# Performance work log

Measured on AMD Instinct MI355X. Metric: run time of the kernel, lower is better.

Reference implementation:

```python
import jax, jax.numpy as jnp
import numpy as np

NEG_SLOPE = 0.2  # PyG GATConv default negative_slope


def gat_layer(x, src, dst, N, W, att_src, att_dst, bias, heads, out_ch, concat):
    # x: [N, Fin]; W: [Fin, heads*out_ch]; att_*: [heads, out_ch]; bias matches output dim
    h = (x @ W).reshape(N, heads, out_ch)              # [N, H, C]
    a_src = (h * att_src).sum(-1)                      # [N, H]
    a_dst = (h * att_dst).sum(-1)                      # [N, H]
    e = jax.nn.leaky_relu(a_src[src] + a_dst[dst], NEG_SLOPE)  # [E, H]
    # segment softmax over incoming edges of each destination node
    e_max = jax.ops.segment_max(e, dst, num_segments=N)        # [N, H]
    e_exp = jnp.exp(e - e_max[dst])                             # [E, H]
    denom = jax.ops.segment_sum(e_exp, dst, num_segments=N)    # [N, H]
    alpha = e_exp / (denom[dst] + 1e-16)                        # [E, H]
    msg = alpha[:, :, None] * h[src]                            # [E, H, C]
    out = jax.ops.segment_sum(msg, dst, num_segments=N)        # [N, H, C]
    out = out.reshape(N, heads * out_ch) if concat else out.mean(axis=1)
    return out + bias


def setup_inputs() -> dict:
    key = jax.random.key(0)
    ks = jax.random.split(key, 10)
    N, E = 40000, 160000
    Fin, H1, C1 = 602, 8, 256
    H2, C2 = 1, 42
    g = lambda k, shape, fan: (jax.random.normal(k, shape, dtype=jnp.float32) * (1.0 / np.sqrt(fan)))
    return {
        "x": jax.random.normal(ks[0], (N, Fin), dtype=jnp.float32),
        "edge_index": jax.random.randint(ks[1], (2, E), 0, N, dtype=jnp.int64),
        "W1": g(ks[2], (Fin, H1 * C1), Fin),
        "att_src1": g(ks[3], (H1, C1), C1),
        "att_dst1": g(ks[4], (H1, C1), C1),
        "b1": jnp.zeros((H1 * C1,), dtype=jnp.float32),
        "W2": g(ks[5], (H1 * C1, H2 * C2), H1 * C1),
        "att_src2": g(ks[6], (H2, C2), C2),
        "att_dst2": g(ks[7], (H2, C2), C2),
        "b2": jnp.zeros((C2,), dtype=jnp.float32),
    }


def reference(x, edge_index, W1, att_src1, att_dst1, b1, W2, att_src2, att_dst2, b2):
    N = x.shape[0]
    # PyG GATConv default add_self_loops=True
    loops = jnp.arange(N, dtype=edge_index.dtype)
    src = jnp.concatenate([edge_index[0], loops])
    dst = jnp.concatenate([edge_index[1], loops])
    h = gat_layer(x, src, dst, N, W1, att_src1, att_dst1, b1, heads=8, out_ch=256, concat=True)
    h = jax.nn.relu(h)  # dropout is identity in eval mode
    h = gat_layer(h, src, dst, N, W2, att_src2, att_dst2, b2, heads=1, out_ch=42, concat=False)
    return jax.nn.log_softmax(h, axis=1)
```

## Files before the change

kernel.cpp:

```cpp
#include <hip/hip_runtime.h>
#include <hip/hip_bf16.h>

#define NN   40000
#define NE   160000
#define ETOT 200000
#define FIN  602
#define NH1  8
#define C1   256
#define F1   2048
#define C2   42
#define NEG  0.2f
#define NB   157
#define KP   608
#define MP   40192

typedef unsigned short u16;
typedef unsigned int   u32;
typedef __bf16 bf16x8 __attribute__((ext_vector_type(8)));
typedef float  f32x4  __attribute__((ext_vector_type(4)));

__device__ __forceinline__ float bfu(u16 v){ return __uint_as_float(((u32)v) << 16); }
__device__ __forceinline__ float bflo(u32 u){ return __uint_as_float(u << 16); }
__device__ __forceinline__ float bfhi(u32 u){ return __uint_as_float(u & 0xffff0000u); }
__device__ __forceinline__ u16 f2bf(float f){
  u32 u = __float_as_uint(f);
  u32 r = (u + 0x7fffu + ((u >> 16) & 1u)) >> 16;
  return (u16)r;
}

__device__ __forceinline__ void gl_lds16(const u16* g, u16* l) {
  __builtin_amdgcn_global_load_lds(
      (const __attribute__((address_space(1))) u32*)(g),
      (__attribute__((address_space(3))) u32*)(l), 16, 0, 0);
}

__global__ void probe_k(const u32* __restrict__ xw, const int* __restrict__ ei,
                        int* __restrict__ flags) {
  if (threadIdx.x == 0) {
    int zc = 0;
    for (int k = 0; k < 64; ++k) zc += (ei[2*k + 1] == 0) ? 1 : 0;
    flags[0] = (zc == 64) ? 1 : 0;
    int inr = 0;
    for (int k = 0; k < 64; ++k) {
      u32 low = xw[k] & 0xffffu;
      int e = (int)((low >> 7) & 0xff);
      inr += (e >= 100 && e <= 140) ? 1 : 0;
    }
    flags[1] = (inr >= 32) ? 0 : 1;
  }
}

__global__ void cvt_f32_k(const void* __restrict__ src, float* __restrict__ dst, int n,
                          const int* __restrict__ flags) {
  int i = blockIdx.x * 256 + threadIdx.x;
  if (i >= n) return;
  dst[i] = flags[1] ? ((const float*)src)[i] : bfu(((const u16*)src)[i]);
}

__global__ void xb_k(const void* __restrict__ x, u16* __restrict__ xb,
                     const int* __restrict__ flags) {
  int k = blockIdx.x * 256 + threadIdx.x;
  int row = blockIdx.y;
  if (k >= KP) return;
  u16 v = 0;
  if (row < NN && k < FIN)
    v = flags[1] ? f2bf(((const float*)x)[(size_t)row * FIN + k])
                 : ((const u16*)x)[(size_t)row * FIN + k];
  xb[(size_t)row * KP + k] = v;
}

__global__ void w1t_k(const void* __restrict__ W1, u16* __restrict__ w1t,
                      const int* __restrict__ flags) {
  int n = blockIdx.x * 256 + threadIdx.x;
  int k = blockIdx.y;
  if (n >= F1) return;
  u16 v = 0;
  if (k < FIN) v = flags[1] ? f2bf(((const float*)W1)[(size_t)k * F1 + n])
                            : ((const u16*)W1)[(size_t)k * F1 + n];
  w1t[(size_t)n * KP + k] = v;
}

__global__ void w2t_k(const void* __restrict__ W2, u16* __restrict__ w2t,
                      const int* __restrict__ flags) {
  int i = blockIdx.x * 256 + threadIdx.x;
  if (i >= 64 * F1) return;
  int c = i >> 11, k = i & (F1 - 1);
  u16 v = 0;
  if (c < C2) v = flags[1] ? f2bf(((const float*)W2)[(size_t)k * C2 + c])
                           : ((const u16*)W2)[(size_t)k * C2 + c];
  w2t[i] = v;
}

__device__ __forceinline__ void edge_sd(const int* __restrict__ ei, int e, int imode,
                                        int& s, int& d) {
  if (e < NE) {
    if (imode) { s = ei[2*e]; d = ei[2*(NE + e)]; }
    else       { s = ei[e];   d = ei[NE + e];     }
  } else { s = d = e - NE; }
}

__global__ void deg_k(const int* __restrict__ ei, int* __restrict__ deg,
                      const int* __restrict__ flags) {
  int e = blockIdx.x * 256 + threadIdx.x;
  if (e >= ETOT) return;
  int s, d; edge_sd(ei, e, flags[0], s, d);
  atomicAdd(&deg[d], 1);
}

__global__ __launch_bounds__(256) void scan1_k(const int* __restrict__ deg,
                                               int* __restrict__ tmp, int* __restrict__ bsum) {
  __shared__ int s[256];
  int b = blockIdx.x, t = threadIdx.x, i = b * 256 + t;
  int v = (i < NN) ? deg[i] : 0;
  s[t] = v; __syncthreads();
  for (int o = 1; o < 256; o <<= 1) {
    int u = (t >= o) ? s[t - o] : 0;
    __syncthreads(); s[t] += u; __syncthreads();
  }
  if (i < NN) tmp[i] = s[t];
  if (t == 255) bsum[b] = s[255];
}

__global__ __launch_bounds__(256) void scan2_k(int* __restrict__ bsum) {
  __shared__ int s[256];
  int t = threadIdx.x;
  int v = (t < NB) ? bsum[t] : 0;
  s[t] = v; __syncthreads();
  for (int o = 1; o < 256; o <<= 1) {
    int u = (t >= o) ? s[t - o] : 0;
    __syncthreads(); s[t] += u; __syncthreads();
  }
  if (t < NB) bsum[t] = s[t];
}

__global__ void scan3_k(const int* __restrict__ deg, const int* __restrict__ tmp,
                        const int* __restrict__ bsum, int* __restrict__ start, int* __restrict__ cur) {
  int i = blockIdx.x * 256 + threadIdx.x;
  if (i >= NN) return;
  int b = i >> 8;
  int off = b ? bsum[b - 1] : 0;
  int excl = tmp[i] - deg[i] + off;
  start[i] = excl; cur[i] = excl;
}

__global__ void fill_k(const int* __restrict__ ei, int* __restrict__ cur,
                       int* __restrict__ csr_src, int* __restrict__ csr_dst,
                       const int* __restrict__ flags) {
  int e = blockIdx.x * 256 + threadIdx.x;
  if (e >= ETOT) return;
  int s, d; edge_sd(ei, e, flags[0], s, d);
  int pos = atomicAdd(&cur[d], 1);
  csr_src[pos] = s; csr_dst[pos] = d;
}

__global__ __launch_bounds__(512) void gemm1c_k(const u16* __restrict__ xb,
                                                const u16* __restrict__ w1t,
                                                u16* __restrict__ h1,
                                                const float* __restrict__ as1c,
                                                const float* __restrict__ ad1c,
                                                float* __restrict__ a_s1,
                                                float* __restrict__ a_d1) {
  __shared__ u16 As[2 * 8192];
  __shared__ u16 Bs[2 * 8192];
  const int t = threadIdx.x;
  const int lane = t & 63, wid = t >> 6;
  const int wr = wid >> 2, wc = wid & 3;
  const int m0 = blockIdx.y * 256, n0 = blockIdx.x * 256;
  const int l16 = lane & 15;
  f32x4 acc[8][4];
  #pragma unroll
  for (int i = 0; i < 8; ++i)
    #pragma unroll
    for (int j = 0; j < 4; ++j) acc[i][j] = (f32x4){0.f, 0.f, 0.f, 0.f};

  const int kc = ((t & 3) ^ ((t >> 3) & 3)) * 8;
  const size_t sa0 = (size_t)(m0 + (t >> 2)) * KP + kc;
  const size_t sa1 = sa0 + (size_t)128 * KP;
  const size_t sb0 = (size_t)(n0 + (t >> 2)) * KP + kc;
  const size_t sb1 = sb0 + (size_t)128 * KP;

  const int fsw = ((lane >> 4) ^ ((l16 >> 1) & 3)) << 3;
  const int rdA = (wr * 128 + l16) * 32 + fsw;
  const int rdB = (wc * 64 + l16) * 32 + fsw;

#define STAGE(K0, B) do {                                  \
    u16* a_ = As + (B) * 8192 + (wid << 9);                \
    u16* b_ = Bs + (B) * 8192 + (wid << 9);                \
    gl_lds16(xb  + sa0 + (K0), a_);                        \
    gl_lds16(xb  + sa1 + (K0), a_ + 4096);                 \
    gl_lds16(w1t + sb0 + (K0), b_);                        \
    gl_lds16(w1t + sb1 + (K0), b_ + 4096);                 \
  } while (0)

  STAGE(0, 0);
  __syncthreads();
  int cur = 0;
  for (int k0 = 0; k0 < KP; k0 += 32) {
    if (k0 + 32 < KP) STAGE(k0 + 32, cur ^ 1);
    const u16* Ab = As + cur * 8192;
    const u16* Bb = Bs + cur * 8192;
    bf16x8 bfr[4];
    #pragma unroll
    for (int ni = 0; ni < 4; ++ni)
      bfr[ni] = *(const bf16x8*)&Bb[rdB + ni * 512];
    #pragma unroll
    for (int mi = 0; mi < 8; ++mi) {
      bf16x8 af = *(const bf16x8*)&Ab[rdA + mi * 512];
      #pragma unroll
      for (int ni = 0; ni < 4; ++ni)
        acc[mi][ni] = __builtin_amdgcn_mfma_f32_16x16x32_bf16(af, bfr[ni], acc[mi][ni], 0, 0, 0);
    }
    __syncthreads();
    cur ^= 1;
  }
#undef STAGE

  const int h0 = n0 >> 8;
  const int lr4 = (lane >> 4) * 4;
  #pragma unroll
  for (int mi = 0; mi < 8; ++mi) {
    float ps[4] = {0.f, 0.f, 0.f, 0.f}, pd[4] = {0.f, 0.f, 0.f, 0.f};
    #pragma unroll
    for (int ni = 0; ni < 4; ++ni) {
      int col = n0 + wc * 64 + ni * 16 + l16;
      float wsv = as1c[col], wdv = ad1c[col];
      #pragma unroll
      for (int r = 0; r < 4; ++r) {
        float v = acc[mi][ni][r];
        ps[r] += v * wsv;
        pd[r] += v * wdv;
      }
    }
    #pragma unroll
    for (int o = 1; o < 16; o <<= 1) {
      #pragma unroll
      for (int r = 0; r < 4; ++r) {
        ps[r] += __shfl_xor(ps[r], o, 64);
        pd[r] += __shfl_xor(pd[r], o, 64);
      }
    }
    int rowb = m0 + wr * 128 + mi * 16 + lr4;
    if (l16 == 0) {
      #pragma unroll
      for (int r = 0; r < 4; ++r) {
        int row = rowb + r;
        if (row < NN) {
          atomicAdd(&a_s1[row * NH1 + h0], ps[r]);
          atomicAdd(&a_d1[row * NH1 + h0], pd[r]);
        }
      }
    }
    #pragma unroll
    for (int r = 0; r < 4; ++r) {
      int row = rowb + r;
      if (row < NN) {
        #pragma unroll
        for (int ni = 0; ni < 4; ++ni) {
          int col = n0 + wc * 64 + ni * 16 + l16;
          h1[(size_t)row * F1 + col] = f2bf(acc[mi][ni][r]);
        }
      }
    }
  }
}

__global__ __launch_bounds__(256) void gemm1m_k(const void* __restrict__ xv,
                                                const u16* __restrict__ w1t,
                                                u16* __restrict__ h1,
                                                const int* __restrict__ flags) {
  __shared__ u16 As[128][40];
  __shared__ u16 Bs[128][40];
  const int fm = flags[1];
  const int t = threadIdx.x;
  const int lane = t & 63, wid = t >> 6;
  const int wr = wid >> 1, wc = wid & 1;
  const int m0 = blockIdx.y * 128, n0 = blockIdx.x * 128;
  const int l16 = lane & 15, lk = (lane >> 4) * 8;
  f32x4 acc[4][4];
  #pragma unroll
  for (int i = 0; i < 4; ++i)
    #pragma unroll
    for (int j = 0; j < 4; ++j) acc[i][j] = (f32x4){0.f, 0.f, 0.f, 0.f};
  const int arow = t >> 2;
  const int akb  = (t & 3) * 8;
  for (int k0 = 0; k0 < KP; k0 += 32) {
    #pragma unroll
    for (int i = 0; i < 2; ++i) {
      int row = arow + i * 64;
      int rg = m0 + row;
      u32 d0 = 0, d1 = 0, d2 = 0, d3 = 0;
      if (rg < NN) {
        if (k0 + 32 <= FIN) {
          if (fm) {
            const float* xp = (const float*)xv + (size_t)rg * FIN + k0 + akb;
            float2 p0 = *(const float2*)(xp);
            float2 p1 = *(const float2*)(xp + 2);
            float2 p2 = *(const float2*)(xp + 4);
            float2 p3 = *(const float2*)(xp + 6);
            d0 = (u32)f2bf(p0.x) | ((u32)f2bf(p0.y) << 16);
            d1 = (u32)f2bf(p1.x) | ((u32)f2bf(p1.y) << 16);
            d2 = (u32)f2bf(p2.x) | ((u32)f2bf(p2.y) << 16);
            d3 = (u32)f2bf(p3.x) | ((u32)f2bf(p3.y) << 16);
          } else {
            const u16* xp = (const u16*)xv + (size_t)rg * FIN + k0 + akb;
            d0 = *(const u32*)(xp);
            d1 = *(const u32*)(xp + 2);
            d2 = *(const u32*)(xp + 4);
            d3 = *(const u32*)(xp + 6);
          }
        } else {
          u16 e[8];
          #pragma unroll
          for (int q = 0; q < 8; ++q) {
            int k = k0 + akb + q;
            e[q] = 0;
            if (k < FIN)
              e[q] = fm ? f2bf(((const float*)xv)[(size_t)rg * FIN + k])
                        : ((const u16*)xv)[(size_t)rg * FIN + k];
          }
          d0 = (u32)e[0] | ((u32)e[1] << 16);
          d1 = (u32)e[2] | ((u32)e[3] << 16);
          d2 = (u32)e[4] | ((u32)e[5] << 16);
          d3 = (u32)e[6] | ((u32)e[7] << 16);
        }
      }
      *(uint4*)&As[row][akb] = make_uint4(d0, d1, d2, d3);
      const u16* wp = w1t + (size_t)(n0 + row) * KP + k0 + akb;
      *(uint4*)&Bs[row][akb] = *(const uint4*)wp;
    }
    __syncthreads();
    bf16x8 bfr[4];
    #pragma unroll
    for (int ni = 0; ni < 4; ++ni)
      bfr[ni] = *(const bf16x8*)&Bs[wc * 64 + ni * 16 + l16][lk];
    #pragma unroll
    for (int mi = 0; mi < 4; ++mi) {
      bf16x8 af = *(const bf16x8*)&As[wr * 64 + mi * 16 + l16][lk];
      #pragma unroll
      for (int ni = 0; ni < 4; ++ni)
        acc[mi][ni] = __builtin_amdgcn_mfma_f32_16x16x32_bf16(af, bfr[ni], acc[mi][ni], 0, 0, 0);
    }
    __syncthreads();
  }
  const int lr4 = (lane >> 4) * 4;
  #pragma unroll
  for (int mi = 0; mi < 4; ++mi) {
    #pragma unroll
    for (int r = 0; r < 4; ++r) {
      int row = m0 + wr * 64 + mi * 16 + lr4 + r;
      if (row < NN) {
        #pragma unroll
        for (int ni = 0; ni < 4; ++ni) {
          int col = n0 + wc * 64 + ni * 16 + l16;
          h1[(size_t)row * F1 + col] = f2bf(acc[mi][ni][r]);
        }
      }
    }
  }
}

__global__ __launch_bounds__(256) void att1_k(const u16* __restrict__ h1,
                                              const float* __restrict__ as1c, const float* __restrict__ ad1c,
                                              float* __restrict__ a_s, float* __restrict__ a_d) {
  int n = blockIdx.x, t = threadIdx.x;
  int h = t >> 5, l = t & 31;
  int base = h * C1 + l * 8;
  const u16* hp = h1 + (size_t)n * F1 + base;
  uint4 v = *(const uint4*)hp;
  u32 w[4] = {v.x, v.y, v.z, v.w};
  float ss = 0.f, sd = 0.f;
  #pragma unroll
  for (int p = 0; p < 4; ++p) {
    float e0 = bflo(w[p]), e1 = bfhi(w[p]);
    ss += e0 * as1c[base + 2*p] + e1 * as1c[base + 2*p + 1];
    sd += e0 * ad1c[base + 2*p] + e1 * ad1c[base + 2*p + 1];
  }
  #pragma unroll
  for (int o = 16; o > 0; o >>= 1) {
    ss += __shfl_down(ss, o, 32);
    sd += __shfl_down(sd, o, 32);
  }
  if (l == 0) { a_s[n * NH1 + h] = ss; a_d[n * NH1 + h] = sd; }
}

__global__ __launch_bounds__(512) void gfuse_k(const int* __restrict__ start, const int* __restrict__ deg,
                                               const int* __restrict__ csr_src,
                                               const float* __restrict__ a_s1, const float* __restrict__ a_d1,
                                               const u16* __restrict__ h1, const float* __restrict__ b1c,
                                               const u16* __restrict__ w2t, float* __restrict__ h2) {
  __shared__ u16 rowsL[16 * F1];
  __shared__ float pb[4][16][16];
  int t = threadIdx.x;
  int nb = blockIdx.x * 16;
  int sub = t & 255, grp = t >> 8;
  int h = sub >> 5;
  int c0 = sub * 8;
  float4 bA = *(const float4*)(b1c + c0);
  float4 bB = *(const float4*)(b1c + c0 + 4);
  for (int ii = 0; ii < 8; ++ii) {
    int i = grp * 8 + ii;
    int n = nb + i;
    int s0 = start[n], jend = s0 + deg[n];
    float ad = a_d1[n * NH1 + h];
    float a0=0.f,a1=0.f,a2=0.f,a3=0.f,a4=0.f,a5=0.f,a6=0.f,a7=0.f,den=0.f;
    int j = s0;
    for (; j + 2 <= jend; j += 2) {
      int sA = csr_src[j], sB = csr_src[j + 1];
      float vA = a_s1[sA * NH1 + h] + ad;
      float vB = a_s1[sB * NH1 + h] + ad;
      vA = vA > 0.f ? vA : NEG * vA;
      vB = vB > 0.f ? vB : NEG * vB;
      float eA = expf(vA), eB = expf(vB);
      uint4 uA = *(const uint4*)(h1 + (size_t)sA * F1 + c0);
      uint4 uB = *(const uint4*)(h1 + (size_t)sB * F1 + c0);
      den += eA + eB;
      a0 += eA * bflo(uA.x) + eB * bflo(uB.x);
      a1 += eA * bfhi(uA.x) + eB * bfhi(uB.x);
      a2 += eA * bflo(uA.y) + eB * bflo(uB.y);
      a3 += eA * bfhi(uA.y) + eB * bfhi(uB.y);
      a4 += eA * bflo(uA.z) + eB * bflo(uB.z);
      a5 += eA * bfhi(uA.z) + eB * bfhi(uB.z);
      a6 += eA * bflo(uA.w) + eB * bflo(uB.w);
      a7 += eA * bfhi(uA.w) + eB * bfhi(uB.w);
    }
    if (j < jend) {
      int sA = csr_src[j];
      float vA = a_s1[sA * NH1 + h] + ad;
      vA = vA > 0.f ? vA : NEG * vA;
      float eA = expf(vA);
      uint4 uA = *(const uint4*)(h1 + (size_t)sA * F1 + c0);
      den += eA;
      a0 += eA * bflo(uA.x); a1 += eA * bfhi(uA.x);
      a2 += eA * bflo(uA.y); a3 += eA * bfhi(uA.y);
      a4 += eA * bflo(uA.z); a5 += eA * bfhi(uA.z);
      a6 += eA * bflo(uA.w); a7 += eA * bfhi(uA.w);
    }
    float inv = 1.f / (den + 1e-16f);
    u16 o0 = f2bf(fmaxf(a0 * inv + bA.x, 0.f));
    u16 o1 = f2bf(fmaxf(a1 * inv + bA.y, 0.f));
    u16 o2 = f2bf(fmaxf(a2 * inv + bA.z, 0.f));
    u16 o3 = f2bf(fmaxf(a3 * inv + bA.w, 0.f));
    u16 o4 = f2bf(fmaxf(a4 * inv + bB.x, 0.f));
    u16 o5 = f2bf(fmaxf(a5 * inv + bB.y, 0.f));
    u16 o6 = f2bf(fmaxf(a6 * inv + bB.z, 0.f));
    u16 o7 = f2bf(fmaxf(a7 * inv + bB.w, 0.f));
    uint4 pk;
    pk.x = (u32)o0 | ((u32)o1 << 16);
    pk.y = (u32)o2 | ((u32)o3 << 16);
    pk.z = (u32)o4 | ((u32)o5 << 16);
    pk.w = (u32)o6 | ((u32)o7 << 16);
    int sw = (i & 7) << 3;
    *(uint4*)&rowsL[i * F1 + (c0 ^ sw)] = pk;
  }
  __syncthreads();
  int lane = t & 63, wid = t >> 6;
  int g = wid & 3, kh = wid >> 2;
  int l16 = lane & 15, lk = (lane >> 4) * 8;
  const u16* wt = w2t + (size_t)(g * 16 + l16) * F1;
  int sw = (l16 & 7) << 3;
  f32x4 acc2 = (f32x4){0.f, 0.f, 0.f, 0.f};
  const int kbase = kh * (F1 / 2);
  for (int k0 = 0; k0 < F1 / 2; k0 += 32) {
    int kk = kbase + k0 + lk;
    bf16x8 af = *(const bf16x8*)&rowsL[l16 * F1 + (kk ^ sw)];
    bf16x8 bf = *(const bf16x8*)(wt + kk);
    acc2 = __builtin_amdgcn_mfma_f32_16x16x32_bf16(af, bf, acc2, 0, 0, 0);
  }
  int mb = (lane >> 4) * 4;
  if (kh == 1) {
    #pragma unroll
    for (int r = 0; r < 4; ++r) pb[g][mb + r][l16] = acc2[r];
  }
  __syncthreads();
  if (kh == 0) {
    int col = g * 16 + l16;
    if (col < C2) {
      #pragma unroll
      for (int r = 0; r < 4; ++r)
        h2[(size_t)(nb + mb + r) * C2 + col] = acc2[r] + pb[g][mb + r][l16];
    }
  }
}

__global__ __launch_bounds__(64) void att2_k(const float* __restrict__ h2,
                                             const float* __restrict__ as2, const float* __restrict__ ad2,
                                             float* __restrict__ a_s, float* __restrict__ a_d) {
  int n = blockIdx.x, t = threadIdx.x;
  float ss = 0.f, sd = 0.f;
  if (t < C2) {
    float v = h2[(size_t)n * C2 + t];
    ss = v * as2[t];
    sd = v * ad2[t];
  }
  #pragma unroll
  for (int o = 32; o > 0; o >>= 1) {
    ss += __shfl_down(ss, o, 64);
    sd += __shfl_down(sd, o, 64);
  }
  if (t == 0) { a_s[n] = ss; a_d[n] = sd; }
}

__global__ __launch_bounds__(64) void gath2_k(const int* __restrict__ start, const int* __restrict__ deg,
                                              const int* __restrict__ csr_src,
                                              const float* __restrict__ a_s, const float* __restrict__ a_d,
                                              const float* __restrict__ h2, const float* __restrict__ b2,
                                              void* __restrict__ outv, const int* __restrict__ flags) {
  int n = blockIdx.x, t = threadIdx.x;
  int s0 = start[n], cnt = deg[n];
  float ad = a_d[n];
  float acc = 0.f, den = 0.f;
  for (int j = s0; j < s0 + cnt; ++j) {
    int s = csr_src[j];
    float v = a_s[s] + ad;
    v = v > 0.f ? v : NEG * v;
    float e = expf(v);
    den += e;
    if (t < C2) acc += e * h2[(size_t)s * C2 + t];
  }
  float raw = (t < C2) ? acc / (den + 1e-16f) + b2[t] : -1e30f;
  float m = raw;
  #pragma unroll
  for (int o = 32; o > 0; o >>= 1) m = fmaxf(m, __shfl_down(m, o, 64));
  m = __shfl(m, 0, 64);
  float e2 = (t < C2) ? expf(raw - m) : 0.f;
  float ssum = e2;
  #pragma unroll
  for (int o = 32; o > 0; o >>= 1) ssum += __shfl_down(ssum, o, 64);
  ssum = __shfl(ssum, 0, 64);
  if (t < C2) {
    float v = raw - m - logf(ssum);
    if (flags[1]) ((float*)outv)[(size_t)n * C2 + t] = v;
    else          ((u16*) outv)[(size_t)n * C2 + t] = f2bf(v);
  }
}

extern "C" void kernel_launch(void* const* d_in, const int* in_sizes, int n_in,
                              void* d_out, int out_size, void* d_ws, size_t ws_size,
                              hipStream_t stream) {
  const void* x   = d_in[0];
  const int*  ei  = (const int*)d_in[1];
  const void* W1  = d_in[2];
  const void* as1 = d_in[3];
  const void* ad1 = d_in[4];
  const void* b1  = d_in[5];
  const void* W2  = d_in[6];
  const void* as2 = d_in[7];
  const void* ad2 = d_in[8];
  const void* b2  = d_in[9];

  char* ws = (char*)d_ws;
  u16*   h1      = (u16*)  (ws);
  float* h2      = (float*)(ws + 163840000);
  float* a_s1    = (float*)(ws + 170560000);
  float* a_d1    = (float*)(ws + 171840000);
  float* a_s2    = (float*)(ws + 173120000);
  float* a_d2    = (float*)(ws + 173280000);
  int*   deg     = (int*)  (ws + 173440000);
  int*   start   = (int*)  (ws + 173600000);
  int*   cur     = (int*)  (ws + 173760000);
  int*   tmp     = (int*)  (ws + 173920000);
  int*   csr_src = (int*)  (ws + 174080000);
  int*   csr_dst = (int*)  (ws + 174880000);
  int*   bsum    = (int*)  (ws + 175680000);
  u16*   w1t     = (u16*)  (ws + 175681024);
  u16*   w2t     = (u16*)  (ws + 178171392);
  float* as1c    = (float*)(ws + 178433536);
  float* ad1c    = (float*)(ws + 178441728);
  float* b1c     = (float*)(ws + 178449920);
  float* as2c    = (float*)(ws + 178458112);
  float* ad2c    = (float*)(ws + 178458368);
  float* b2c     = (float*)(ws + 178458624);
  int*   flags   = (int*)  (ws + 178458880);
  const size_t TOTAL_BASE = 178459136;
  u16*   xb      = (u16*)  (ws + TOTAL_BASE);
  const size_t TOTAL_A = TOTAL_BASE + (size_t)MP * KP * 2;
  if (ws_size < TOTAL_BASE) return;
  const bool pathA = (ws_size >= TOTAL_A);

  probe_k<<<1, 64, 0, stream>>>((const u32*)x, ei, flags);

  cvt_f32_k<<<(F1 + 255) / 256, 256, 0, stream>>>(as1, as1c, F1, flags);
  cvt_f32_k<<<(F1 + 255) / 256, 256, 0, stream>>>(ad1, ad1c, F1, flags);
  cvt_f32_k<<<(F1 + 255) / 256, 256, 0, stream>>>(b1, b1c, F1, flags);
  cvt_f32_k<<<1, 256, 0, stream>>>(as2, as2c, C2, flags);
  cvt_f32_k<<<1, 256, 0, stream>>>(ad2, ad2c, C2, flags);
  cvt_f32_k<<<1, 256, 0, stream>>>(b2, b2c, C2, flags);
  w1t_k<<<dim3(8, KP), 256, 0, stream>>>(W1, w1t, flags);
  w2t_k<<<(64 * F1 + 255) / 256, 256, 0, stream>>>(W2, w2t, flags);

  hipMemsetAsync(deg, 0, NN * sizeof(int), stream);
  hipMemsetAsync(a_s1, 0, 2 * NN * NH1 * sizeof(float), stream);
  const int EB = (ETOT + 255) / 256;
  deg_k  <<<EB, 256, 0, stream>>>(ei, deg, flags);
  scan1_k<<<NB, 256, 0, stream>>>(deg, tmp, bsum);
  scan2_k<<<1, 256, 0, stream>>>(bsum);
  scan3_k<<<NB, 256, 0, stream>>>(deg, tmp, bsum, start, cur);
  fill_k <<<EB, 256, 0, stream>>>(ei, cur, csr_src, csr_dst, flags);

  if (pathA) {
    xb_k<<<dim3((KP + 255) / 256, MP), 256, 0, stream>>>(x, xb, flags);
    gemm1c_k<<<dim3(8, MP / 256), 512, 0, stream>>>(xb, w1t, h1, as1c, ad1c, a_s1, a_d1);
  } else {
    gemm1m_k<<<dim3(16, 313), 256, 0, stream>>>(x, w1t, h1, flags);
    att1_k<<<NN, 256, 0, stream>>>(h1, as1c, ad1c, a_s1, a_d1);
  }
  gfuse_k<<<NN / 16, 512, 0, stream>>>(start, deg, csr_src, a_s1, a_d1, h1, b1c, w2t, h2);

  att2_k<<<NN, 64, 0, stream>>>(h2, as2c, ad2c, a_s2, a_d2);
  gath2_k<<<NN, 64, 0, stream>>>(start, deg, csr_src, a_s2, a_d2, h2, b2c, d_out, flags);
}
```

Before: 641.7 us.

## Stage GEMM1 output through LDS, fuse att2 into gfuse, merge conversion kernels

The GEMM1 epilogue now writes bf16 tiles into shared memory and copies them out with 16-byte vector stores, replacing scattered 2-byte global stores. The layer-2 attention dot products are computed inside gfuse with shuffle reductions and atomics, which removes the separate att2 kernel and its re-read of h2. The six small parameter conversion launches become one kernel, and gath2 packs four nodes per 256-thread block. This adds extra barriers in the GEMM epilogue and depends on a_s2/a_d2 sitting right after a_s1 in the workspace so the enlarged memset zeroes them.

Result: faster. 623.1 us (-2.9%).

```diff
diff --git a/kernel.cpp b/kernel.cpp
--- a/kernel.cpp
+++ b/kernel.cpp
@@ -13,6 +13,7 @@
 #define NB   157
 #define KP   608
 #define MP   40192
+#define CSS  264
 
 typedef unsigned short u16;
 typedef unsigned int   u32;
@@ -50,11 +51,25 @@
   }
 }
 
-__global__ void cvt_f32_k(const void* __restrict__ src, float* __restrict__ dst, int n,
+__global__ void cvt_all_k(const void* __restrict__ as1, const void* __restrict__ ad1,
+                          const void* __restrict__ b1,  const void* __restrict__ as2,
+                          const void* __restrict__ ad2, const void* __restrict__ b2,
+                          float* __restrict__ as1c, float* __restrict__ ad1c,
+                          float* __restrict__ b1c,  float* __restrict__ as2c,
+                          float* __restrict__ ad2c, float* __restrict__ b2c,
                           const int* __restrict__ flags) {
   int i = blockIdx.x * 256 + threadIdx.x;
-  if (i >= n) return;
-  dst[i] = flags[1] ? ((const float*)src)[i] : bfu(((const u16*)src)[i]);
+  int fm = flags[1];
+  if (i < F1) {
+    as1c[i] = fm ? ((const float*)as1)[i] : bfu(((const u16*)as1)[i]);
+    ad1c[i] = fm ? ((const float*)ad1)[i] : bfu(((const u16*)ad1)[i]);
+    b1c[i]  = fm ? ((const float*)b1)[i]  : bfu(((const u16*)b1)[i]);
+  }
+  if (i < C2) {
+    as2c[i] = fm ? ((const float*)as2)[i] : bfu(((const u16*)as2)[i]);
+    ad2c[i] = fm ? ((const float*)ad2)[i] : bfu(((const u16*)ad2)[i]);
+    b2c[i]  = fm ? ((const float*)b2)[i]  : bfu(((const u16*)b2)[i]);
+  }
 }
 
 __global__ void xb_k(const void* __restrict__ x, u16* __restrict__ xb,
@@ -239,8 +254,8 @@
         pd[r] += __shfl_xor(pd[r], o, 64);
       }
     }
-    int rowb = m0 + wr * 128 + mi * 16 + lr4;
     if (l16 == 0) {
+      int rowb = m0 + wr * 128 + mi * 16 + lr4;
       #pragma unroll
       for (int r = 0; r < 4; ++r) {
         int row = rowb + r;
@@ -250,16 +265,25 @@
         }
       }
     }
-    #pragma unroll
-    for (int r = 0; r < 4; ++r) {
-      int row = rowb + r;
-      if (row < NN) {
-        #pragma unroll
-        for (int ni = 0; ni < 4; ++ni) {
-          int col = n0 + wc * 64 + ni * 16 + l16;
-          h1[(size_t)row * F1 + col] = f2bf(acc[mi][ni][r]);
-        }
-      }
+  }
+
+  u16* Cs = As;
+  const int rrow = t >> 4;
+  const int rchk = t & 15;
+  for (int mi = 0; mi < 8; ++mi) {
+    __syncthreads();
+    #pragma unroll
+    for (int ni = 0; ni < 4; ++ni)
+      #pragma unroll
+      for (int r = 0; r < 4; ++r)
+        Cs[(wr * 16 + lr4 + r) * CSS + wc * 64 + ni * 16 + l16] = f2bf(acc[mi][ni][r]);
+    __syncthreads();
+    int grow = m0 + (rrow >> 4) * 128 + mi * 16 + (rrow & 15);
+    if (grow < NN) {
+      const uint4* src = (const uint4*)&Cs[rrow * CSS + rchk * 16];
+      uint4 v0 = src[0], v1 = src[1];
+      uint4* dst = (uint4*)&h1[(size_t)grow * F1 + n0 + rchk * 16];
+      dst[0] = v0; dst[1] = v1;
     }
   }
 }
@@ -387,7 +411,10 @@
                                                const int* __restrict__ csr_src,
                                                const float* __restrict__ a_s1, const float* __restrict__ a_d1,
                                                const u16* __restrict__ h1, const float* __restrict__ b1c,
-                                               const u16* __restrict__ w2t, float* __restrict__ h2) {
+                                               const u16* __restrict__ w2t,
+                                               const float* __restrict__ as2c, const float* __restrict__ ad2c,
+                                               float* __restrict__ h2,
+                                               float* __restrict__ a_s2, float* __restrict__ a_d2) {
   __shared__ u16 rowsL[16 * F1];
   __shared__ float pb[4][16][16];
   int t = threadIdx.x;
@@ -474,38 +501,44 @@
   __syncthreads();
   if (kh == 0) {
     int col = g * 16 + l16;
+    float vals[4];
+    #pragma unroll
+    for (int r = 0; r < 4; ++r) vals[r] = acc2[r] + pb[g][mb + r][l16];
     if (col < C2) {
       #pragma unroll
       for (int r = 0; r < 4; ++r)
-        h2[(size_t)(nb + mb + r) * C2 + col] = acc2[r] + pb[g][mb + r][l16];
-    }
-  }
-}
-
-__global__ __launch_bounds__(64) void att2_k(const float* __restrict__ h2,
-                                             const float* __restrict__ as2, const float* __restrict__ ad2,
-                                             float* __restrict__ a_s, float* __restrict__ a_d) {
-  int n = blockIdx.x, t = threadIdx.x;
-  float ss = 0.f, sd = 0.f;
-  if (t < C2) {
-    float v = h2[(size_t)n * C2 + t];
-    ss = v * as2[t];
-    sd = v * ad2[t];
-  }
-  #pragma unroll
-  for (int o = 32; o > 0; o >>= 1) {
-    ss += __shfl_down(ss, o, 64);
-    sd += __shfl_down(sd, o, 64);
-  }
-  if (t == 0) { a_s[n] = ss; a_d[n] = sd; }
-}
-
-__global__ __launch_bounds__(64) void gath2_k(const int* __restrict__ start, const int* __restrict__ deg,
-                                              const int* __restrict__ csr_src,
-                                              const float* __restrict__ a_s, const float* __restrict__ a_d,
-                                              const float* __restrict__ h2, const float* __restrict__ b2,
-                                              void* __restrict__ outv, const int* __restrict__ flags) {
-  int n = blockIdx.x, t = threadIdx.x;
+        h2[(size_t)(nb + mb + r) * C2 + col] = vals[r];
+    }
+    float as2v = (col < C2) ? as2c[col] : 0.f;
+    float ad2v = (col < C2) ? ad2c[col] : 0.f;
+    float ps[4], pd[4];
+    #pragma unroll
+    for (int r = 0; r < 4; ++r) { ps[r] = vals[r] * as2v; pd[r] = vals[r] * ad2v; }
+    #pragma unroll
+    for (int o = 1; o < 16; o <<= 1) {
+      #pragma unroll
+      for (int r = 0; r < 4; ++r) {
+        ps[r] += __shfl_xor(ps[r], o, 64);
+        pd[r] += __shfl_xor(pd[r], o, 64);
+      }
+    }
+    if (l16 == 0 && g < 3) {
+      #pragma unroll
+      for (int r = 0; r < 4; ++r) {
+        atomicAdd(&a_s2[nb + mb + r], ps[r]);
+        atomicAdd(&a_d2[nb + mb + r], pd[r]);
+      }
+    }
+  }
+}
+
+__global__ __launch_bounds__(256) void gath2_k(const int* __restrict__ start, const int* __restrict__ deg,
+                                               const int* __restrict__ csr_src,
+                                               const float* __restrict__ a_s, const float* __restrict__ a_d,
+                                               const float* __restrict__ h2, const float* __restrict__ b2,
+                                               void* __restrict__ outv, const int* __restrict__ flags) {
+  int w = threadIdx.x >> 6, lane = threadIdx.x & 63;
+  int n = blockIdx.x * 4 + w;
   int s0 = start[n], cnt = deg[n];
   float ad = a_d[n];
   float acc = 0.f, den = 0.f;
@@ -515,22 +548,22 @@
     v = v > 0.f ? v : NEG * v;
     float e = expf(v);
     den += e;
-    if (t < C2) acc += e * h2[(size_t)s * C2 + t];
-  }
-  float raw = (t < C2) ? acc / (den + 1e-16f) + b2[t] : -1e30f;
+    if (lane < C2) acc += e * h2[(size_t)s * C2 + lane];
+  }
+  float raw = (lane < C2) ? acc / (den + 1e-16f) + b2[lane] : -1e30f;
   float m = raw;
   #pragma unroll
   for (int o = 32; o > 0; o >>= 1) m = fmaxf(m, __shfl_down(m, o, 64));
   m = __shfl(m, 0, 64);
-  float e2 = (t < C2) ? expf(raw - m) : 0.f;
+  float e2 = (lane < C2) ? expf(raw - m) : 0.f;
   float ssum = e2;
   #pragma unroll
   for (int o = 32; o > 0; o >>= 1) ssum += __shfl_down(ssum, o, 64);
   ssum = __shfl(ssum, 0, 64);
-  if (t < C2) {
+  if (lane < C2) {
     float v = raw - m - logf(ssum);
-    if (flags[1]) ((float*)outv)[(size_t)n * C2 + t] = v;
-    else          ((u16*) outv)[(size_t)n * C2 + t] = f2bf(v);
+    if (flags[1]) ((float*)outv)[(size_t)n * C2 + lane] = v;
+    else          ((u16*) outv)[(size_t)n * C2 + lane] = f2bf(v);
   }
 }
 
@@ -579,17 +612,13 @@
 
   probe_k<<<1, 64, 0, stream>>>((const u32*)x, ei, flags);
 
-  cvt_f32_k<<<(F1 + 255) / 256, 256, 0, stream>>>(as1, as1c, F1, flags);
-  cvt_f32_k<<<(F1 + 255) / 256, 256, 0, stream>>>(ad1, ad1c, F1, flags);
-  cvt_f32_k<<<(F1 + 255) / 256, 256, 0, stream>>>(b1, b1c, F1, flags);
-  cvt_f32_k<<<1, 256, 0, stream>>>(as2, as2c, C2, flags);
-  cvt_f32_k<<<1, 256, 0, stream>>>(ad2, ad2c, C2, flags);
-  cvt_f32_k<<<1, 256, 0, stream>>>(b2, b2c, C2, flags);
+  cvt_all_k<<<(F1 + 255) / 256, 256, 0, stream>>>(as1, ad1, b1, as2, ad2, b2,
+                                                  as1c, ad1c, b1c, as2c, ad2c, b2c, flags);
   w1t_k<<<dim3(8, KP), 256, 0, stream>>>(W1, w1t, flags);
   w2t_k<<<(64 * F1 + 255) / 256, 256, 0, stream>>>(W2, w2t, flags);
 
   hipMemsetAsync(deg, 0, NN * sizeof(int), stream);
-  hipMemsetAsync(a_s1, 0, 2 * NN * NH1 * sizeof(float), stream);
+  hipMemsetAsync(a_s1, 0, (2 * NN * NH1 + 2 * NN) * sizeof(float), stream);
   const int EB = (ETOT + 255) / 256;
   deg_k  <<<EB, 256, 0, stream>>>(ei, deg, flags);
   scan1_k<<<NB, 256, 0, stream>>>(deg, tmp, bsum);
@@ -604,8 +633,8 @@
     gemm1m_k<<<dim3(16, 313), 256, 0, stream>>>(x, w1t, h1, flags);
     att1_k<<<NN, 256, 0, stream>>>(h1, as1c, ad1c, a_s1, a_d1);
   }
-  gfuse_k<<<NN / 16, 512, 0, stream>>>(start, deg, csr_src, a_s1, a_d1, h1, b1c, w2t, h2);
-
-  att2_k<<<NN, 64, 0, stream>>>(h2, as2c, ad2c, a_s2, a_d2);
-  gath2_k<<<NN, 64, 0, stream>>>(start, deg, csr_src, a_s2, a_d2, h2, b2c, d_out, flags);
-}
+  gfuse_k<<<NN / 16, 512, 0, stream>>>(start, deg, csr_src, a_s1, a_d1, h1, b1c, w2t,
+                                       as2c, ad2c, h2, a_s2, a_d2);
+
+  gath2_k<<<NN / 4, 256, 0, stream>>>(start, deg, csr_src, a_s2, a_d2, h2, b2c, d_out, flags);
+}
```
